# Kernel optimization log

Hardware: AMD Instinct MI355X
Metric: run time of the kernel (lower is better)

Reference implementation:

```python
import jax, jax.numpy as jnp
import numpy as np

# Model config (matches init_kwargs)
V, SMAX, D, DH, H, M, L = 32000, 512, 512, 64, 8, 2048, 6
B, S, T = 4, 512, 512
PAD = 0

_SPEC = [
    ("tok_emb", (V, D), "n"), ("pos_emb", (SMAX, D), "n"),
    ("enc_ln1_w", (L, D), "1"), ("enc_ln1_b", (L, D), "0"),
    ("enc_wq", (L, H, D, DH), "n"), ("enc_wk", (L, H, D, DH), "n"), ("enc_wv", (L, H, D, DH), "n"),
    ("enc_wo", (L, H * DH, D), "n"), ("enc_bo", (L, D), "0"),
    ("enc_ln2_w", (L, D), "1"), ("enc_ln2_b", (L, D), "0"),
    ("enc_w1", (L, D, M), "n"), ("enc_b1", (L, M), "0"),
    ("enc_w2", (L, M, D), "n"), ("enc_b2", (L, D), "0"),
    ("enc_lnf_w", (D,), "1"), ("enc_lnf_b", (D,), "0"),
    ("dec_ln1_w", (L, D), "1"), ("dec_ln1_b", (L, D), "0"),
    ("dec_wq_s", (L, H, D, DH), "n"), ("dec_wk_s", (L, H, D, DH), "n"), ("dec_wv_s", (L, H, D, DH), "n"),
    ("dec_wo_s", (L, H * DH, D), "n"), ("dec_bo_s", (L, D), "0"),
    ("dec_ln2_w", (L, D), "1"), ("dec_ln2_b", (L, D), "0"),
    ("dec_wq_c", (L, H, D, DH), "n"), ("dec_wk_c", (L, H, D, DH), "n"), ("dec_wv_c", (L, H, D, DH), "n"),
    ("dec_wo_c", (L, H * DH, D), "n"), ("dec_bo_c", (L, D), "0"),
    ("dec_ln3_w", (L, D), "1"), ("dec_ln3_b", (L, D), "0"),
    ("dec_w1", (L, D, M), "n"), ("dec_b1", (L, M), "0"),
    ("dec_w2", (L, M, D), "n"), ("dec_b2", (L, D), "0"),
    ("dec_lnf_w", (D,), "1"), ("dec_lnf_b", (D,), "0"),
    ("head_w", (D, V), "n"), ("head_b", (V,), "0"),
]


def setup_inputs() -> dict:
    key = jax.random.key(0)
    k1, k2, key = jax.random.split(key, 3)
    inp = {
        "tokens_source": jax.random.randint(k1, (B, S), 0, V),
        "tokens_destination": jax.random.randint(k2, (B, T), 0, V),
    }
    for name, shape, kind in _SPEC:
        if kind == "n":
            key, k = jax.random.split(key)
            inp[name] = jax.random.normal(k, shape, jnp.float32) * 0.02
        elif kind == "1":
            inp[name] = jnp.ones(shape, jnp.float32)
        else:
            inp[name] = jnp.zeros(shape, jnp.float32)
    return inp


def _ln(x, w, b):
    mu = x.mean(-1, keepdims=True)
    var = ((x - mu) ** 2).mean(-1, keepdims=True)
    return (x - mu) * jax.lax.rsqrt(var + 1e-5) * w + b


def _mha(xq, xkv, wq, wk, wv, wo, bo, mask):
    # wq/wk/wv: [H, D, dh]; wo: [H*dh, D]; mask: bool [B or 1, Sq, Sk] (broadcast over heads)
    q = jnp.einsum("bsd,hde->bhse", xq, wq)
    k = jnp.einsum("btd,hde->bhte", xkv, wk)
    v = jnp.einsum("btd,hde->bhte", xkv, wv)
    scores = jnp.einsum("bhse,bhte->bhst", q, k) / (DH ** 0.5)
    scores = jnp.where(mask[:, None], scores, -jnp.inf)
    w = jax.nn.softmax(scores, axis=-1)
    o = jnp.einsum("bhst,bhte->bhse", w, v)
    b_, _, s_, _ = o.shape
    o = o.transpose(0, 2, 1, 3).reshape(b_, s_, H * DH)  # concat heads (head 0 first)
    return o @ wo + bo


def _forward(src, dst, p):
    s_, t_ = src.shape[1], dst.shape[1]
    key_mask = (src != PAD)[:, None, :]                      # [B,1,S]: mask over source keys
    causal = jnp.tril(jnp.ones((t_, t_), bool))[None]        # [1,T,T]
    x = p["tok_emb"][src] + p["pos_emb"][:s_]
    for i in range(L):
        h = _ln(x, p["enc_ln1_w"][i], p["enc_ln1_b"][i])
        x = x + _mha(h, h, p["enc_wq"][i], p["enc_wk"][i], p["enc_wv"][i], p["enc_wo"][i], p["enc_bo"][i], key_mask)
        h = _ln(x, p["enc_ln2_w"][i], p["enc_ln2_b"][i])
        x = x + jax.nn.gelu(h @ p["enc_w1"][i] + p["enc_b1"][i], approximate=False) @ p["enc_w2"][i] + p["enc_b2"][i]
    xe = _ln(x, p["enc_lnf_w"], p["enc_lnf_b"])
    y = p["tok_emb"][dst] + p["pos_emb"][:t_]
    for i in range(L):
        h = _ln(y, p["dec_ln1_w"][i], p["dec_ln1_b"][i])
        y = y + _mha(h, h, p["dec_wq_s"][i], p["dec_wk_s"][i], p["dec_wv_s"][i], p["dec_wo_s"][i], p["dec_bo_s"][i], causal)
        h = _ln(y, p["dec_ln2_w"][i], p["dec_ln2_b"][i])
        y = y + _mha(h, xe, p["dec_wq_c"][i], p["dec_wk_c"][i], p["dec_wv_c"][i], p["dec_wo_c"][i], p["dec_bo_c"][i], key_mask)
        h = _ln(y, p["dec_ln3_w"][i], p["dec_ln3_b"][i])
        y = y + jax.nn.gelu(h @ p["dec_w1"][i] + p["dec_b1"][i], approximate=False) @ p["dec_w2"][i] + p["dec_b2"][i]
    yd = _ln(y, p["dec_lnf_w"], p["dec_lnf_b"])
    return yd @ p["head_w"] + p["head_b"]  # logits [B, T, V]


def reference(tokens_source, tokens_destination, tok_emb, pos_emb, enc_ln1_w, enc_ln1_b, enc_wq, enc_wk, enc_wv, enc_wo, enc_bo, enc_ln2_w, enc_ln2_b, enc_w1, enc_b1, enc_w2, enc_b2, enc_lnf_w, enc_lnf_b, dec_ln1_w, dec_ln1_b, dec_wq_s, dec_wk_s, dec_wv_s, dec_wo_s, dec_bo_s, dec_ln2_w, dec_ln2_b, dec_wq_c, dec_wk_c, dec_wv_c, dec_wo_c, dec_bo_c, dec_ln3_w, dec_ln3_b, dec_w1, dec_b1, dec_w2, dec_b2, dec_lnf_w, dec_lnf_b, head_w, head_b):
    p = {k: v for k, v in locals().items() if k not in ("tokens_source", "tokens_destination")}
    return _forward(tokens_source, tokens_destination, p)
```

## Files before the change

kernel.cpp:

```cpp
#include <hip/hip_runtime.h>
#include <math.h>


typedef __bf16 bf16;
typedef bf16  bf16x8 __attribute__((ext_vector_type(8)));
typedef float f32x4  __attribute__((ext_vector_type(4)));

#define DEV __device__ __forceinline__

DEV f32x4 mfma16(bf16x8 a, bf16x8 b, f32x4 c) {
  return __builtin_amdgcn_mfma_f32_16x16x32_bf16(a, b, c, 0, 0, 0);
}

DEV void async_copy16(const bf16* g, bf16* l) {
  __builtin_amdgcn_global_load_lds(
      (__attribute__((address_space(1))) void*)(g),
      (__attribute__((address_space(3))) void*)(l), 16, 0, 0);
}

__global__ __launch_bounds__(256) void tcast_kernel(
    const float* __restrict__ in, bf16* __restrict__ out, const int R, const int C,
    const long long oHi, const long long oLo, const int zdiv, const long long oOfs)
{
  __shared__ float tile[32][33];
  const int z = blockIdx.z;
  const long long zi = (long long)z * R * C;
  const long long zo = (long long)(z / zdiv) * oHi + (long long)(z % zdiv) * oLo + oOfs;
  const int c0 = blockIdx.x * 32, r0 = blockIdx.y * 32;
  const int tx = threadIdx.x, ty = threadIdx.y;
#pragma unroll
  for (int i = 0; i < 32; i += 8)
    tile[ty + i][tx] = in[zi + (long long)(r0 + ty + i) * C + c0 + tx];
  __syncthreads();
#pragma unroll
  for (int i = 0; i < 32; i += 8)
    out[zo + (long long)(c0 + ty + i) * R + r0 + tx] = (bf16)tile[tx][ty + i];
}

__global__ __launch_bounds__(128) void embed_kernel(
    const int* __restrict__ tok, const float* __restrict__ temb,
    const float* __restrict__ pemb, float* __restrict__ x)
{
  const int row  = blockIdx.x;
  const int sPos = row & 511;
  const int t    = tok[row];
  const int d    = threadIdx.x * 4;
  f32x4 a = *(const f32x4*)&temb[(long long)t * 512 + d];
  f32x4 p = *(const f32x4*)&pemb[(long long)sPos * 512 + d];
  *(f32x4*)&x[(long long)row * 512 + d] = a + p;
}

__global__ __launch_bounds__(64) void ln_kernel(
    const float* __restrict__ x, const float* __restrict__ w,
    const float* __restrict__ b, bf16* __restrict__ out)
{
  const int row = blockIdx.x;
  const int lane = threadIdx.x;
  const float* xr = x + (long long)row * 512;
  f32x4 a0 = *(const f32x4*)&xr[lane * 8];
  f32x4 a1 = *(const f32x4*)&xr[lane * 8 + 4];
  float s = 0.f, q = 0.f;
#pragma unroll
  for (int k = 0; k < 4; ++k) { s += a0[k] + a1[k]; q += a0[k]*a0[k] + a1[k]*a1[k]; }
#pragma unroll
  for (int m = 1; m < 64; m <<= 1) { s += __shfl_xor(s, m); q += __shfl_xor(q, m); }
  const float mean = s * (1.f / 512.f);
  const float var  = q * (1.f / 512.f) - mean * mean;
  const float rs   = rsqrtf(var + 1e-5f);
  f32x4 w0 = *(const f32x4*)&w[lane * 8], w1 = *(const f32x4*)&w[lane * 8 + 4];
  f32x4 b0 = *(const f32x4*)&b[lane * 8], b1 = *(const f32x4*)&b[lane * 8 + 4];
  bf16x8 o;
#pragma unroll
  for (int k = 0; k < 4; ++k) {
    o[k]     = (bf16)((a0[k] - mean) * rs * w0[k] + b0[k]);
    o[k + 4] = (bf16)((a1[k] - mean) * rs * w1[k] + b1[k]);
  }
  *(bf16x8*)&out[(long long)row * 512 + lane * 8] = o;
}

__global__ __launch_bounds__(256) void addln_kernel(
    const bf16* __restrict__ g, const float* __restrict__ bias,
    float* __restrict__ x, const float* __restrict__ w,
    const float* __restrict__ bb, bf16* __restrict__ out)
{
  const int row  = blockIdx.x * 4 + (threadIdx.x >> 6);
  const int lane = threadIdx.x & 63;
  const int c0   = lane * 8;
  float* xr = x + (long long)row * 512;
  f32x4 a0 = *(const f32x4*)&xr[c0];
  f32x4 a1 = *(const f32x4*)&xr[c0 + 4];
  bf16x8 gv = *(const bf16x8*)&g[(long long)row * 512 + c0];
  f32x4 bi0 = *(const f32x4*)&bias[c0], bi1 = *(const f32x4*)&bias[c0 + 4];
  float v[8];
#pragma unroll
  for (int k = 0; k < 4; ++k) {
    v[k]     = a0[k] + (float)gv[k]     + bi0[k];
    v[k + 4] = a1[k] + (float)gv[k + 4] + bi1[k];
  }
  *(f32x4*)&xr[c0]     = f32x4{v[0], v[1], v[2], v[3]};
  *(f32x4*)&xr[c0 + 4] = f32x4{v[4], v[5], v[6], v[7]};
  float s = 0.f, q = 0.f;
#pragma unroll
  for (int k = 0; k < 8; ++k) { s += v[k]; q += v[k] * v[k]; }
#pragma unroll
  for (int m = 1; m < 64; m <<= 1) { s += __shfl_xor(s, m); q += __shfl_xor(q, m); }
  const float mean = s * (1.f / 512.f);
  const float var  = q * (1.f / 512.f) - mean * mean;
  const float rs   = rsqrtf(var + 1e-5f);
  f32x4 w0 = *(const f32x4*)&w[c0], w1 = *(const f32x4*)&w[c0 + 4];
  f32x4 b0 = *(const f32x4*)&bb[c0], b1 = *(const f32x4*)&bb[c0 + 4];
  bf16x8 o;
#pragma unroll
  for (int k = 0; k < 4; ++k) {
    o[k]     = (bf16)((v[k] - mean) * rs * w0[k] + b0[k]);
    o[k + 4] = (bf16)((v[k + 4] - mean) * rs * w1[k] + b1[k]);
  }
  *(bf16x8*)&out[(long long)row * 512 + c0] = o;
}

template <int MODE>
__global__ __launch_bounds__(256) void attn_kernel(
    const bf16* __restrict__ Q, const bf16* __restrict__ K,
    const bf16* __restrict__ Vt, bf16* __restrict__ O,
    const int* __restrict__ srctok)
{
  __shared__ bf16 Qs[64 * 72];
  __shared__ bf16 Ks[128 * 72];
  __shared__ bf16 Vs[64 * 136];
  __shared__ bf16 Ps[4 * 16 * 132];
  __shared__ float Ms[512];

  const int bh = blockIdx.y;
  const int b  = bh >> 3;
  const int q0 = blockIdx.x * 64;
  const int tid = threadIdx.x;
  const int wv = tid >> 6, ln = tid & 63;
  const int lr = ln & 15, g = ln >> 4;
  const bf16* Qg = Q + ((long long)bh * 512 + q0) * 64;
  const bf16* Kg = K + (long long)bh * 512 * 64;
  const bf16* Vg = Vt + (long long)bh * 64 * 512;

  for (int i = tid; i < 512; i += 256) {
    const int r = i >> 3, c = (i & 7) * 8;
    *(uint4*)&Qs[r * 72 + c] = *(const uint4*)&Qg[r * 64 + c];
  }
  if (MODE == 0) {
    for (int i = tid; i < 512; i += 256)
      Ms[i] = (srctok[b * 512 + i] != 0) ? 0.f : -1e30f;
  }

  float m[4] = {-1e30f, -1e30f, -1e30f, -1e30f};
  float l[4] = {0.f, 0.f, 0.f, 0.f};
  f32x4 o[4] = {};

  const int ktEnd = (MODE == 1) ? (q0 + 64) : 512;
  bf16* Pw = Ps + wv * (16 * 132);

  for (int kt = 0; kt < ktEnd; kt += 128) {
    __syncthreads();
    for (int i = tid; i < 1024; i += 256) {
      const int r = i >> 3, c = (i & 7) * 8;
      *(uint4*)&Ks[r * 72 + c] = *(const uint4*)&Kg[(long long)(kt + r) * 64 + c];
    }
    for (int i = tid; i < 1024; i += 256) {
      const int r = i >> 4, c = (i & 15) * 8;
      *(uint4*)&Vs[r * 136 + c] = *(const uint4*)&Vg[(long long)r * 512 + kt + c];
    }
    __syncthreads();

    f32x4 sf[8] = {};
#pragma unroll
    for (int s = 0; s < 2; ++s) {
      const bf16x8 aq = *(const bf16x8*)&Qs[(wv * 16 + lr) * 72 + s * 32 + g * 8];
#pragma unroll
      for (int j = 0; j < 8; ++j) {
        const bf16x8 bk = *(const bf16x8*)&Ks[(j * 16 + lr) * 72 + s * 32 + g * 8];
        sf[j] = mfma16(aq, bk, sf[j]);
      }
    }
    float rm[4] = {-1e30f, -1e30f, -1e30f, -1e30f};
#pragma unroll
    for (int j = 0; j < 8; ++j) {
      if (MODE == 0) {
        const float ma = Ms[kt + j * 16 + lr];
#pragma unroll
        for (int r = 0; r < 4; ++r) sf[j][r] += ma;
      } else {
        const int key = kt + j * 16 + lr;
#pragma unroll
        for (int r = 0; r < 4; ++r) {
          const int qq = q0 + wv * 16 + g * 4 + r;
          if (key > qq) sf[j][r] = -1e30f;
        }
      }
#pragma unroll
      for (int r = 0; r < 4; ++r) rm[r] = fmaxf(rm[r], sf[j][r]);
    }
#pragma unroll
    for (int mk = 1; mk < 16; mk <<= 1)
#pragma unroll
      for (int r = 0; r < 4; ++r) rm[r] = fmaxf(rm[r], __shfl_xor(rm[r], mk));
    float al[4], ps[4] = {0.f, 0.f, 0.f, 0.f};
#pragma unroll
    for (int r = 0; r < 4; ++r) {
      const float mx = fmaxf(m[r], rm[r]);
      al[r] = __expf(m[r] - mx);
      m[r] = mx;
    }
#pragma unroll
    for (int j = 0; j < 8; ++j) {
#pragma unroll
      for (int r = 0; r < 4; ++r) {
        const float p = __expf(sf[j][r] - m[r]);
        ps[r] += p;
        Pw[(g * 4 + r) * 132 + j * 16 + lr] = (bf16)p;
      }
    }
#pragma unroll
    for (int mk = 1; mk < 16; mk <<= 1)
#pragma unroll
      for (int r = 0; r < 4; ++r) ps[r] += __shfl_xor(ps[r], mk);
#pragma unroll
    for (int r = 0; r < 4; ++r) l[r] = l[r] * al[r] + ps[r];
#pragma unroll
    for (int n = 0; n < 4; ++n)
#pragma unroll
      for (int r = 0; r < 4; ++r) o[n][r] *= al[r];
#pragma unroll
    for (int ks = 0; ks < 4; ++ks) {
      const bf16x8 ap = *(const bf16x8*)&Pw[lr * 132 + ks * 32 + g * 8];
#pragma unroll
      for (int n = 0; n < 4; ++n) {
        const bf16x8 bv = *(const bf16x8*)&Vs[(n * 16 + lr) * 136 + ks * 32 + g * 8];
        o[n] = mfma16(ap, bv, o[n]);
      }
    }
  }

#pragma unroll
  for (int r = 0; r < 4; ++r) {
    const float inv = 1.f / l[r];
    const long long gr = (long long)b * 512 + q0 + wv * 16 + g * 4 + r;
#pragma unroll
    for (int n = 0; n < 4; ++n)
      O[gr * 512 + (bh & 7) * 64 + n * 16 + lr] = (bf16)(o[n][r] * inv);
  }
}

template <int BM, int BN, int EPI>
__global__ __launch_bounds__(256) void gemm_kernel(
    const bf16* __restrict__ A, const bf16* __restrict__ Bw,
    void* __restrict__ Cc, const float* __restrict__ bias,
    const int K, const int lda, const int ldb, const int ldc,
    const long long sAz, const long long sBz,
    const long long sClo, const long long sChi, const int HB,
    const float scale)
{
  constexpr int BK = 64;
  __shared__ bf16 As[BM * BK];
  __shared__ bf16 Bs[BN * BK];
  constexpr int AISS = (BM * BK * 2) / 4096;
  constexpr int BISS = (BN * BK * 2) / 4096;

  const int z = blockIdx.z;
  const bf16* Az = A + (long long)z * sAz;
  const bf16* Bz = Bw + (long long)z * sBz;
  const long long cofs = (long long)(z % HB) * sClo + (long long)(z / HB) * sChi;

  const int tid  = threadIdx.x;
  const int wave = tid >> 6;
  const int lane = tid & 63;
  const int lr   = lane & 15;
  const int kg   = lane >> 4;

  const int m0 = blockIdx.x * BM;
  const int n0 = blockIdx.y * BN;

  constexpr int FM = BM / 32;
  constexpr int FN = BN / 32;
  const int wm = (wave >> 1) * (BM / 2);
  const int wn = (wave & 1) * (BN / 2);

  f32x4 acc[FM][FN] = {};

  for (int kt = 0; kt < K; kt += BK) {
#pragma unroll
    for (int i = 0; i < AISS; ++i) {
      const int o = i * 4096 + tid * 16;
      const int r = o >> 7;
      const int c = (o & 127) >> 1;
      async_copy16(Az + (long long)(m0 + r) * lda + kt + c, (bf16*)((char*)As + o));
    }
#pragma unroll
    for (int i = 0; i < BISS; ++i) {
      const int o = i * 4096 + tid * 16;
      const int r = o >> 7;
      const int c = (o & 127) >> 1;
      async_copy16(Bz + (long long)(n0 + r) * ldb + kt + c, (bf16*)((char*)Bs + o));
    }
    __syncthreads();
#pragma unroll
    for (int ks = 0; ks < 2; ++ks) {
      bf16x8 af[FM], bq[FN];
#pragma unroll
      for (int i = 0; i < FM; ++i)
        af[i] = *(const bf16x8*)&As[(wm + i * 16 + lr) * BK + ks * 32 + kg * 8];
#pragma unroll
      for (int j = 0; j < FN; ++j)
        bq[j] = *(const bf16x8*)&Bs[(wn + j * 16 + lr) * BK + ks * 32 + kg * 8];
#pragma unroll
      for (int i = 0; i < FM; ++i)
#pragma unroll
        for (int j = 0; j < FN; ++j)
          acc[i][j] = mfma16(af[i], bq[j], acc[i][j]);
    }
    __syncthreads();
  }

#pragma unroll
  for (int i = 0; i < FM; ++i) {
#pragma unroll
    for (int j = 0; j < FN; ++j) {
      const int gc = n0 + wn + j * 16 + lr;
#pragma unroll
      for (int r = 0; r < 4; ++r) {
        const int gr = m0 + wm + i * 16 + kg * 4 + r;
        const float v = acc[i][j][r];
        if constexpr (EPI == 0) {
          ((bf16*)Cc + cofs)[(long long)gr * ldc + gc] = (bf16)v;
        } else if constexpr (EPI == 3) {
          float t = v + bias[gc];
          t = 0.5f * t * (1.f + erff(t * 0.70710678118654752f));
          ((bf16*)Cc)[(long long)gr * ldc + gc] = (bf16)t;
        } else if constexpr (EPI == 4) {
          ((float*)Cc)[(long long)gr * ldc + gc] = v + bias[gc];
        } else if constexpr (EPI == 7) {
          const int sel = (gc >> 9) + (int)sClo;
          const int hh = (gc >> 6) & 7, ee = gc & 63;
          const int bb = gr >> 9, ss = gr & 511;
          bf16* base = (bf16*)Cc + (long long)sel * (2048 * 512);
          const float vv = (sel == 0) ? v * 0.125f : v;
          if (sel < 2) base[(((long long)(bb * 8 + hh) << 9) + ss) * 64 + ee] = (bf16)vv;
          else         base[(((long long)(bb * 8 + hh) << 6) + ee) * 512 + ss] = (bf16)vv;
        }
      }
    }
  }
}

extern "C" void kernel_launch(void* const* d_in, const int* in_sizes, int n_in,
                              void* d_out, int out_size, void* d_ws, size_t ws_size,
                              hipStream_t stream)
{
  const int*   tok_src   = (const int*)d_in[0];
  const int*   tok_dst   = (const int*)d_in[1];
  const float* tok_emb   = (const float*)d_in[2];
  const float* pos_emb   = (const float*)d_in[3];
  const float* enc_ln1_w = (const float*)d_in[4];
  const float* enc_ln1_b = (const float*)d_in[5];
  const float* enc_wq    = (const float*)d_in[6];
  const float* enc_wk    = (const float*)d_in[7];
  const float* enc_wv    = (const float*)d_in[8];
  const float* enc_wo    = (const float*)d_in[9];
  const float* enc_bo    = (const float*)d_in[10];
  const float* enc_ln2_w = (const float*)d_in[11];
  const float* enc_ln2_b = (const float*)d_in[12];
  const float* enc_w1    = (const float*)d_in[13];
  const float* enc_b1    = (const float*)d_in[14];
  const float* enc_w2    = (const float*)d_in[15];
  const float* enc_b2    = (const float*)d_in[16];
  const float* enc_lnf_w = (const float*)d_in[17];
  const float* enc_lnf_b = (const float*)d_in[18];
  const float* dec_ln1_w = (const float*)d_in[19];
  const float* dec_ln1_b = (const float*)d_in[20];
  const float* dec_wq_s  = (const float*)d_in[21];
  const float* dec_wk_s  = (const float*)d_in[22];
  const float* dec_wv_s  = (const float*)d_in[23];
  const float* dec_wo_s  = (const float*)d_in[24];
  const float* dec_bo_s  = (const float*)d_in[25];
  const float* dec_ln2_w = (const float*)d_in[26];
  const float* dec_ln2_b = (const float*)d_in[27];
  const float* dec_wq_c  = (const float*)d_in[28];
  const float* dec_wk_c  = (const float*)d_in[29];
  const float* dec_wv_c  = (const float*)d_in[30];
  const float* dec_wo_c  = (const float*)d_in[31];
  const float* dec_bo_c  = (const float*)d_in[32];
  const float* dec_ln3_w = (const float*)d_in[33];
  const float* dec_ln3_b = (const float*)d_in[34];
  const float* dec_w1    = (const float*)d_in[35];
  const float* dec_b1    = (const float*)d_in[36];
  const float* dec_w2    = (const float*)d_in[37];
  const float* dec_b2    = (const float*)d_in[38];
  const float* dec_lnf_w = (const float*)d_in[39];
  const float* dec_lnf_b = (const float*)d_in[40];
  const float* head_w    = (const float*)d_in[41];
  const float* head_b    = (const float*)d_in[42];
  float* outp = (float*)d_out;

  char* wp = (char*)d_ws;
  auto alloc = [&](size_t nbytes) -> char* {
    char* p = wp; wp += (nbytes + 255) & ~(size_t)255; return p;
  };
  const long long LQKV = 1536LL * 512;
  const long long LKV  = 1024LL * 512;
  const long long LSQ  = 512LL * 512;
  const long long LFF  = 2048LL * 512;

  bf16* tQKV_e = (bf16*)alloc((size_t)6 * LQKV * 2);
  bf16* tQKV_s = (bf16*)alloc((size_t)6 * LQKV * 2);
  bf16* tQ_c   = (bf16*)alloc((size_t)6 * LSQ * 2);
  bf16* tKV_c  = (bf16*)alloc((size_t)6 * LKV * 2);
  bf16* tWo_e  = (bf16*)alloc((size_t)6 * LSQ * 2);
  bf16* tWo_s  = (bf16*)alloc((size_t)6 * LSQ * 2);
  bf16* tWo_c  = (bf16*)alloc((size_t)6 * LSQ * 2);
  bf16* tW1_e  = (bf16*)alloc((size_t)6 * LFF * 2);
  bf16* tW2_e  = (bf16*)alloc((size_t)6 * LFF * 2);
  bf16* tW1_d  = (bf16*)alloc((size_t)6 * LFF * 2);
  bf16* tW2_d  = (bf16*)alloc((size_t)6 * LFF * 2);
  bf16* tHead  = (bf16*)alloc((size_t)32000 * 512 * 2);

  float* x   = (float*)alloc((size_t)2048 * 512 * 4);
  float* y   = (float*)alloc((size_t)2048 * 512 * 4);
  bf16*  h   = (bf16*)alloc((size_t)2048 * 512 * 2);
  bf16*  qkv = (bf16*)alloc((size_t)3 * 2048 * 512 * 2);
  bf16*  xe  = (bf16*)alloc((size_t)2048 * 512 * 2);
  bf16*  ob  = (bf16*)alloc((size_t)2048 * 512 * 2);
  bf16*  t0  = (bf16*)alloc((size_t)2048 * 512 * 2);
  bf16*  h1  = (bf16*)alloc((size_t)2048 * 2048 * 2);
  bf16*  yd  = (bf16*)alloc((size_t)2048 * 512 * 2);

  bf16* ql = qkv;
  bf16* kl = qkv + 2048 * 512;
  bf16* vt = qkv + 2 * 2048 * 512;

  const dim3 tb(32, 8);
  tcast_kernel<<<dim3(2, 16, 48), tb, 0, stream>>>(enc_wq, tQKV_e, 512, 64, LQKV, 32768, 8, 0);
  tcast_kernel<<<dim3(2, 16, 48), tb, 0, stream>>>(enc_wk, tQKV_e, 512, 64, LQKV, 32768, 8, 262144);
  tcast_kernel<<<dim3(2, 16, 48), tb, 0, stream>>>(enc_wv, tQKV_e, 512, 64, LQKV, 32768, 8, 524288);
  tcast_kernel<<<dim3(2, 16, 48), tb, 0, stream>>>(dec_wq_s, tQKV_s, 512, 64, LQKV, 32768, 8, 0);
  tcast_kernel<<<dim3(2, 16, 48), tb, 0, stream>>>(dec_wk_s, tQKV_s, 512, 64, LQKV, 32768, 8, 262144);
  tcast_kernel<<<dim3(2, 16, 48), tb, 0, stream>>>(dec_wv_s, tQKV_s, 512, 64, LQKV, 32768, 8, 524288);
  tcast_kernel<<<dim3(2, 16, 48), tb, 0, stream>>>(dec_wq_c, tQ_c, 512, 64, LSQ, 32768, 8, 0);
  tcast_kernel<<<dim3(2, 16, 48), tb, 0, stream>>>(dec_wk_c, tKV_c, 512, 64, LKV, 32768, 8, 0);
  tcast_kernel<<<dim3(2, 16, 48), tb, 0, stream>>>(dec_wv_c, tKV_c, 512, 64, LKV, 32768, 8, 262144);
  tcast_kernel<<<dim3(16, 16, 6), tb, 0, stream>>>(enc_wo, tWo_e, 512, 512, LSQ, 0, 1, 0);
  tcast_kernel<<<dim3(16, 16, 6), tb, 0, stream>>>(dec_wo_s, tWo_s, 512, 512, LSQ, 0, 1, 0);
  tcast_kernel<<<dim3(16, 16, 6), tb, 0, stream>>>(dec_wo_c, tWo_c, 512, 512, LSQ, 0, 1, 0);
  tcast_kernel<<<dim3(64, 16, 6), tb, 0, stream>>>(enc_w1, tW1_e, 512, 2048, LFF, 0, 1, 0);
  tcast_kernel<<<dim3(16, 64, 6), tb, 0, stream>>>(enc_w2, tW2_e, 2048, 512, LFF, 0, 1, 0);
  tcast_kernel<<<dim3(64, 16, 6), tb, 0, stream>>>(dec_w1, tW1_d, 512, 2048, LFF, 0, 1, 0);
  tcast_kernel<<<dim3(16, 64, 6), tb, 0, stream>>>(dec_w2, tW2_d, 2048, 512, LFF, 0, 1, 0);
  tcast_kernel<<<dim3(1000, 16, 1), tb, 0, stream>>>(head_w, tHead, 512, 32000, 0, 0, 1, 0);

  embed_kernel<<<2048, 128, 0, stream>>>(tok_src, tok_emb, pos_emb, x);
  ln_kernel<<<2048, 64, 0, stream>>>(x, enc_ln1_w, enc_ln1_b, h);
  for (int l = 0; l < 6; ++l) {
    gemm_kernel<128, 128, 7><<<dim3(16, 12, 1), 256, 0, stream>>>(
        h, tQKV_e + (size_t)l * LQKV, qkv, nullptr, 512, 512, 512, 0, 0, 0, 0, 0, 1, 1.f);
    attn_kernel<0><<<dim3(8, 32), 256, 0, stream>>>(ql, kl, vt, ob, tok_src);
    gemm_kernel<64, 64, 0><<<dim3(32, 8, 1), 256, 0, stream>>>(
        ob, tWo_e + (size_t)l * LSQ, t0, nullptr, 512, 512, 512, 512, 0, 0, 0, 0, 1, 1.f);
    addln_kernel<<<512, 256, 0, stream>>>(t0, enc_bo + l * 512, x,
        enc_ln2_w + l * 512, enc_ln2_b + l * 512, h);
    gemm_kernel<128, 128, 3><<<dim3(16, 16, 1), 256, 0, stream>>>(
        h, tW1_e + (size_t)l * LFF, h1, enc_b1 + l * 2048, 512, 512, 512, 2048, 0, 0, 0, 0, 1, 1.f);
    gemm_kernel<64, 64, 0><<<dim3(32, 8, 1), 256, 0, stream>>>(
        h1, tW2_e + (size_t)l * LFF, t0, nullptr, 2048, 2048, 2048, 512, 0, 0, 0, 0, 1, 1.f);
    const float* nw = (l < 5) ? enc_ln1_w + (l + 1) * 512 : enc_lnf_w;
    const float* nb = (l < 5) ? enc_ln1_b + (l + 1) * 512 : enc_lnf_b;
    addln_kernel<<<512, 256, 0, stream>>>(t0, enc_b2 + l * 512, x, nw, nb, (l < 5) ? h : xe);
  }

  embed_kernel<<<2048, 128, 0, stream>>>(tok_dst, tok_emb, pos_emb, y);
  ln_kernel<<<2048, 64, 0, stream>>>(y, dec_ln1_w, dec_ln1_b, h);
  for (int l = 0; l < 6; ++l) {
    gemm_kernel<128, 128, 7><<<dim3(16, 12, 1), 256, 0, stream>>>(
        h, tQKV_s + (size_t)l * LQKV, qkv, nullptr, 512, 512, 512, 0, 0, 0, 0, 0, 1, 1.f);
    attn_kernel<1><<<dim3(8, 32), 256, 0, stream>>>(ql, kl, vt, ob, nullptr);
    gemm_kernel<64, 64, 0><<<dim3(32, 8, 1), 256, 0, stream>>>(
        ob, tWo_s + (size_t)l * LSQ, t0, nullptr, 512, 512, 512, 512, 0, 0, 0, 0, 1, 1.f);
    addln_kernel<<<512, 256, 0, stream>>>(t0, dec_bo_s + l * 512, y,
        dec_ln2_w + l * 512, dec_ln2_b + l * 512, h);
    gemm_kernel<64, 64, 7><<<dim3(32, 8, 1), 256, 0, stream>>>(
        h, tQ_c + (size_t)l * LSQ, qkv, nullptr, 512, 512, 512, 0, 0, 0, 0, 0, 1, 1.f);
    gemm_kernel<128, 128, 7><<<dim3(16, 8, 1), 256, 0, stream>>>(
        xe, tKV_c + (size_t)l * LKV, qkv, nullptr, 512, 512, 512, 0, 0, 0, 1, 0, 1, 1.f);
    attn_kernel<0><<<dim3(8, 32), 256, 0, stream>>>(ql, kl, vt, ob, tok_src);
    gemm_kernel<64, 64, 0><<<dim3(32, 8, 1), 256, 0, stream>>>(
        ob, tWo_c + (size_t)l * LSQ, t0, nullptr, 512, 512, 512, 512, 0, 0, 0, 0, 1, 1.f);
    addln_kernel<<<512, 256, 0, stream>>>(t0, dec_bo_c + l * 512, y,
        dec_ln3_w + l * 512, dec_ln3_b + l * 512, h);
    gemm_kernel<128, 128, 3><<<dim3(16, 16, 1), 256, 0, stream>>>(
        h, tW1_d + (size_t)l * LFF, h1, dec_b1 + l * 2048, 512, 512, 512, 2048, 0, 0, 0, 0, 1, 1.f);
    gemm_kernel<64, 64, 0><<<dim3(32, 8, 1), 256, 0, stream>>>(
        h1, tW2_d + (size_t)l * LFF, t0, nullptr, 2048, 2048, 2048, 512, 0, 0, 0, 0, 1, 1.f);
    const float* nw = (l < 5) ? dec_ln1_w + (l + 1) * 512 : dec_lnf_w;
    const float* nb = (l < 5) ? dec_ln1_b + (l + 1) * 512 : dec_lnf_b;
    addln_kernel<<<512, 256, 0, stream>>>(t0, dec_b2 + l * 512, y, nw, nb, (l < 5) ? h : yd);
  }
  gemm_kernel<128, 128, 4><<<dim3(16, 250, 1), 256, 0, stream>>>(
      yd, tHead, outp, head_b, 512, 512, 512, 32000, 0, 0, 0, 0, 1, 1.f);
}
```

Baseline: 2.366 ms.

## Batch weight casts, fuse embed+LN, hoist cross-attn KV, retile attention

```diff
diff --git a/kernel.cpp b/kernel.cpp
--- a/kernel.cpp
+++ b/kernel.cpp
@@ -18,47 +18,55 @@
       (__attribute__((address_space(3))) void*)(l), 16, 0, 0);
 }
 
-__global__ __launch_bounds__(256) void tcast_kernel(
-    const float* __restrict__ in, bf16* __restrict__ out, const int R, const int C,
-    const long long oHi, const long long oLo, const int zdiv, const long long oOfs)
+struct TJob { const float* in; bf16* out; long long oHi, oLo, oOfs; int R, C, zdiv, tile0; };
+struct TJobs { TJob j[17]; };
+
+__global__ __launch_bounds__(256) void tcast_all(TJobs JJ, int njobs)
 {
   __shared__ float tile[32][33];
-  const int z = blockIdx.z;
-  const long long zi = (long long)z * R * C;
-  const long long zo = (long long)(z / zdiv) * oHi + (long long)(z % zdiv) * oLo + oOfs;
-  const int c0 = blockIdx.x * 32, r0 = blockIdx.y * 32;
-  const int tx = threadIdx.x, ty = threadIdx.y;
+  const int t = blockIdx.x;
+  int ji = 0;
+#pragma unroll
+  for (int k = 1; k < 17; ++k) if (k < njobs && JJ.j[k].tile0 <= t) ji = k;
+  const TJob J = JJ.j[ji];
+  const int rel  = t - J.tile0;
+  const int ntx  = J.C >> 5, nty = J.R >> 5;
+  const int perz = ntx * nty;
+  const int z    = rel / perz;
+  const int r2   = rel - z * perz;
+  const int bx   = r2 % ntx, by = r2 / ntx;
+
+  const long long zi = (long long)z * J.R * J.C;
+  const long long zo = (long long)(z / J.zdiv) * J.oHi + (long long)(z % J.zdiv) * J.oLo + J.oOfs;
+  const int c0 = bx * 32, r0 = by * 32;
+  const int tx = threadIdx.x & 31, ty = (threadIdx.x >> 5);
 #pragma unroll
   for (int i = 0; i < 32; i += 8)
-    tile[ty + i][tx] = in[zi + (long long)(r0 + ty + i) * C + c0 + tx];
+    tile[ty + i][tx] = J.in[zi + (long long)(r0 + ty + i) * J.C + c0 + tx];
   __syncthreads();
 #pragma unroll
   for (int i = 0; i < 32; i += 8)
-    out[zo + (long long)(c0 + ty + i) * R + r0 + tx] = (bf16)tile[tx][ty + i];
-}
-
-__global__ __launch_bounds__(128) void embed_kernel(
+    J.out[zo + (long long)(c0 + ty + i) * J.R + r0 + tx] = (bf16)tile[tx][ty + i];
+}
+
+__global__ __launch_bounds__(64) void embedln_kernel(
     const int* __restrict__ tok, const float* __restrict__ temb,
-    const float* __restrict__ pemb, float* __restrict__ x)
+    const float* __restrict__ pemb, float* __restrict__ x,
+    const float* __restrict__ w, const float* __restrict__ b,
+    bf16* __restrict__ out)
 {
   const int row  = blockIdx.x;
   const int sPos = row & 511;
   const int t    = tok[row];
-  const int d    = threadIdx.x * 4;
-  f32x4 a = *(const f32x4*)&temb[(long long)t * 512 + d];
-  f32x4 p = *(const f32x4*)&pemb[(long long)sPos * 512 + d];
-  *(f32x4*)&x[(long long)row * 512 + d] = a + p;
-}
-
-__global__ __launch_bounds__(64) void ln_kernel(
-    const float* __restrict__ x, const float* __restrict__ w,
-    const float* __restrict__ b, bf16* __restrict__ out)
-{
-  const int row = blockIdx.x;
   const int lane = threadIdx.x;
-  const float* xr = x + (long long)row * 512;
-  f32x4 a0 = *(const f32x4*)&xr[lane * 8];
-  f32x4 a1 = *(const f32x4*)&xr[lane * 8 + 4];
+  const int c0   = lane * 8;
+  f32x4 a0 = *(const f32x4*)&temb[(long long)t * 512 + c0];
+  f32x4 a1 = *(const f32x4*)&temb[(long long)t * 512 + c0 + 4];
+  f32x4 p0 = *(const f32x4*)&pemb[(long long)sPos * 512 + c0];
+  f32x4 p1 = *(const f32x4*)&pemb[(long long)sPos * 512 + c0 + 4];
+  a0 += p0; a1 += p1;
+  *(f32x4*)&x[(long long)row * 512 + c0]     = a0;
+  *(f32x4*)&x[(long long)row * 512 + c0 + 4] = a1;
   float s = 0.f, q = 0.f;
 #pragma unroll
   for (int k = 0; k < 4; ++k) { s += a0[k] + a1[k]; q += a0[k]*a0[k] + a1[k]*a1[k]; }
@@ -67,15 +75,15 @@
   const float mean = s * (1.f / 512.f);
   const float var  = q * (1.f / 512.f) - mean * mean;
   const float rs   = rsqrtf(var + 1e-5f);
-  f32x4 w0 = *(const f32x4*)&w[lane * 8], w1 = *(const f32x4*)&w[lane * 8 + 4];
-  f32x4 b0 = *(const f32x4*)&b[lane * 8], b1 = *(const f32x4*)&b[lane * 8 + 4];
+  f32x4 w0 = *(const f32x4*)&w[c0], w1 = *(const f32x4*)&w[c0 + 4];
+  f32x4 b0 = *(const f32x4*)&b[c0], b1 = *(const f32x4*)&b[c0 + 4];
   bf16x8 o;
 #pragma unroll
   for (int k = 0; k < 4; ++k) {
     o[k]     = (bf16)((a0[k] - mean) * rs * w0[k] + b0[k]);
     o[k + 4] = (bf16)((a1[k] - mean) * rs * w1[k] + b1[k]);
   }
-  *(bf16x8*)&out[(long long)row * 512 + lane * 8] = o;
+  *(bf16x8*)&out[(long long)row * 512 + c0] = o;
 }
 
 __global__ __launch_bounds__(256) void addln_kernel(
@@ -119,79 +127,51 @@
 }
 
 template <int MODE>
-__global__ __launch_bounds__(256) void attn_kernel(
+__global__ __launch_bounds__(64) void attn_kernel(
     const bf16* __restrict__ Q, const bf16* __restrict__ K,
     const bf16* __restrict__ Vt, bf16* __restrict__ O,
     const int* __restrict__ srctok)
 {
-  __shared__ bf16 Qs[64 * 72];
-  __shared__ bf16 Ks[128 * 72];
-  __shared__ bf16 Vs[64 * 136];
-  __shared__ bf16 Ps[4 * 16 * 132];
-  __shared__ float Ms[512];
-
+  __shared__ bf16 Pw[16 * 68];
   const int bh = blockIdx.y;
   const int b  = bh >> 3;
-  const int q0 = blockIdx.x * 64;
-  const int tid = threadIdx.x;
-  const int wv = tid >> 6, ln = tid & 63;
+  const int q0 = blockIdx.x * 16;
+  const int ln = threadIdx.x;
   const int lr = ln & 15, g = ln >> 4;
   const bf16* Qg = Q + ((long long)bh * 512 + q0) * 64;
   const bf16* Kg = K + (long long)bh * 512 * 64;
   const bf16* Vg = Vt + (long long)bh * 64 * 512;
-
-  for (int i = tid; i < 512; i += 256) {
-    const int r = i >> 3, c = (i & 7) * 8;
-    *(uint4*)&Qs[r * 72 + c] = *(const uint4*)&Qg[r * 64 + c];
-  }
-  if (MODE == 0) {
-    for (int i = tid; i < 512; i += 256)
-      Ms[i] = (srctok[b * 512 + i] != 0) ? 0.f : -1e30f;
-  }
+  const int* tkb = srctok + b * 512;
+
+  const bf16x8 aq0 = *(const bf16x8*)&Qg[lr * 64 + g * 8];
+  const bf16x8 aq1 = *(const bf16x8*)&Qg[lr * 64 + 32 + g * 8];
 
   float m[4] = {-1e30f, -1e30f, -1e30f, -1e30f};
   float l[4] = {0.f, 0.f, 0.f, 0.f};
   f32x4 o[4] = {};
 
-  const int ktEnd = (MODE == 1) ? (q0 + 64) : 512;
-  bf16* Pw = Ps + wv * (16 * 132);
-
-  for (int kt = 0; kt < ktEnd; kt += 128) {
-    __syncthreads();
-    for (int i = tid; i < 1024; i += 256) {
-      const int r = i >> 3, c = (i & 7) * 8;
-      *(uint4*)&Ks[r * 72 + c] = *(const uint4*)&Kg[(long long)(kt + r) * 64 + c];
-    }
-    for (int i = tid; i < 1024; i += 256) {
-      const int r = i >> 4, c = (i & 15) * 8;
-      *(uint4*)&Vs[r * 136 + c] = *(const uint4*)&Vg[(long long)r * 512 + kt + c];
-    }
-    __syncthreads();
-
-    f32x4 sf[8] = {};
-#pragma unroll
-    for (int s = 0; s < 2; ++s) {
-      const bf16x8 aq = *(const bf16x8*)&Qs[(wv * 16 + lr) * 72 + s * 32 + g * 8];
-#pragma unroll
-      for (int j = 0; j < 8; ++j) {
-        const bf16x8 bk = *(const bf16x8*)&Ks[(j * 16 + lr) * 72 + s * 32 + g * 8];
-        sf[j] = mfma16(aq, bk, sf[j]);
-      }
+  const int ktEnd = (MODE == 1) ? (q0 + 16) : 512;
+  for (int kt = 0; kt < ktEnd; kt += 64) {
+    f32x4 sf[4] = {};
+#pragma unroll
+    for (int j = 0; j < 4; ++j) {
+      const bf16x8 bk0 = *(const bf16x8*)&Kg[(long long)(kt + j * 16 + lr) * 64 + g * 8];
+      const bf16x8 bk1 = *(const bf16x8*)&Kg[(long long)(kt + j * 16 + lr) * 64 + 32 + g * 8];
+      sf[j] = mfma16(aq0, bk0, sf[j]);
+      sf[j] = mfma16(aq1, bk1, sf[j]);
     }
     float rm[4] = {-1e30f, -1e30f, -1e30f, -1e30f};
 #pragma unroll
-    for (int j = 0; j < 8; ++j) {
+    for (int j = 0; j < 4; ++j) {
       if (MODE == 0) {
-        const float ma = Ms[kt + j * 16 + lr];
-#pragma unroll
-        for (int r = 0; r < 4; ++r) sf[j][r] += ma;
+        const bool ok = (tkb[kt + j * 16 + lr] != 0);
+#pragma unroll
+        for (int r = 0; r < 4; ++r) if (!ok) sf[j][r] = -1e30f;
       } else {
         const int key = kt + j * 16 + lr;
 #pragma unroll
-        for (int r = 0; r < 4; ++r) {
-          const int qq = q0 + wv * 16 + g * 4 + r;
-          if (key > qq) sf[j][r] = -1e30f;
-        }
+        for (int r = 0; r < 4; ++r)
+          if (key > q0 + g * 4 + r) sf[j][r] = -1e30f;
       }
 #pragma unroll
       for (int r = 0; r < 4; ++r) rm[r] = fmaxf(rm[r], sf[j][r]);
@@ -208,12 +188,12 @@
       m[r] = mx;
     }
 #pragma unroll
-    for (int j = 0; j < 8; ++j) {
+    for (int j = 0; j < 4; ++j) {
 #pragma unroll
       for (int r = 0; r < 4; ++r) {
-        const float p = __expf(sf[j][r] - m[r]);
+        const float p = (sf[j][r] <= -1e29f) ? 0.f : __expf(sf[j][r] - m[r]);
         ps[r] += p;
-        Pw[(g * 4 + r) * 132 + j * 16 + lr] = (bf16)p;
+        Pw[(g * 4 + r) * 68 + j * 16 + lr] = (bf16)p;
       }
     }
 #pragma unroll
@@ -227,11 +207,11 @@
 #pragma unroll
       for (int r = 0; r < 4; ++r) o[n][r] *= al[r];
 #pragma unroll
-    for (int ks = 0; ks < 4; ++ks) {
-      const bf16x8 ap = *(const bf16x8*)&Pw[lr * 132 + ks * 32 + g * 8];
+    for (int ks = 0; ks < 2; ++ks) {
+      const bf16x8 ap = *(const bf16x8*)&Pw[lr * 68 + ks * 32 + g * 8];
 #pragma unroll
       for (int n = 0; n < 4; ++n) {
-        const bf16x8 bv = *(const bf16x8*)&Vs[(n * 16 + lr) * 136 + ks * 32 + g * 8];
+        const bf16x8 bv = *(const bf16x8*)&Vg[(long long)(n * 16 + lr) * 512 + kt + ks * 32 + g * 8];
         o[n] = mfma16(ap, bv, o[n]);
       }
     }
@@ -240,14 +220,14 @@
 #pragma unroll
   for (int r = 0; r < 4; ++r) {
     const float inv = 1.f / l[r];
-    const long long gr = (long long)b * 512 + q0 + wv * 16 + g * 4 + r;
+    const long long gr = (long long)b * 512 + q0 + g * 4 + r;
 #pragma unroll
     for (int n = 0; n < 4; ++n)
       O[gr * 512 + (bh & 7) * 64 + n * 16 + lr] = (bf16)(o[n][r] * inv);
   }
 }
 
-template <int BM, int BN, int EPI>
+template <int BM, int BN, int EPI, bool SWZ = false>
 __global__ __launch_bounds__(256) void gemm_kernel(
     const bf16* __restrict__ A, const bf16* __restrict__ Bw,
     void* __restrict__ Cc, const float* __restrict__ bias,
@@ -273,8 +253,17 @@
   const int lr   = lane & 15;
   const int kg   = lane >> 4;
 
-  const int m0 = blockIdx.x * BM;
-  const int n0 = blockIdx.y * BN;
+  int bx = blockIdx.x, by = blockIdx.y;
+  if constexpr (SWZ) {
+    const int nx = gridDim.x;
+    const int nwg = nx * gridDim.y;
+    const int id = by * nx + bx;
+    const int chunk = nwg >> 3;
+    const int swz = (id & 7) * chunk + (id >> 3);
+    bx = swz % nx; by = swz / nx;
+  }
+  const int m0 = bx * BM;
+  const int n0 = by * BN;
 
   constexpr int FM = BM / 32;
   constexpr int FN = BN / 32;
@@ -333,15 +322,22 @@
           t = 0.5f * t * (1.f + erff(t * 0.70710678118654752f));
           ((bf16*)Cc)[(long long)gr * ldc + gc] = (bf16)t;
         } else if constexpr (EPI == 4) {
-          ((float*)Cc)[(long long)gr * ldc + gc] = v + bias[gc];
+          __builtin_nontemporal_store(v + bias[gc], &((float*)Cc)[(long long)gr * ldc + gc]);
         } else if constexpr (EPI == 7) {
-          const int sel = (gc >> 9) + (int)sClo;
+          const int sel = gc >> 9;
           const int hh = (gc >> 6) & 7, ee = gc & 63;
           const int bb = gr >> 9, ss = gr & 511;
           bf16* base = (bf16*)Cc + (long long)sel * (2048 * 512);
           const float vv = (sel == 0) ? v * 0.125f : v;
           if (sel < 2) base[(((long long)(bb * 8 + hh) << 9) + ss) * 64 + ee] = (bf16)vv;
           else         base[(((long long)(bb * 8 + hh) << 6) + ee) * 512 + ss] = (bf16)vv;
+        } else if constexpr (EPI == 8) {
+          const int sel = gc >> 9;
+          const int hh = (gc >> 6) & 7, ee = gc & 63;
+          const int bb = gr >> 9, ss = gr & 511;
+          bf16* base = (bf16*)Cc + (long long)z * sChi + (long long)sel * (2048 * 512);
+          if (sel == 0) base[(((long long)(bb * 8 + hh) << 9) + ss) * 64 + ee] = (bf16)v;
+          else          base[(((long long)(bb * 8 + hh) << 6) + ee) * 512 + ss] = (bf16)v;
         }
       }
     }
@@ -405,6 +401,7 @@
   const long long LKV  = 1024LL * 512;
   const long long LSQ  = 512LL * 512;
   const long long LFF  = 2048LL * 512;
+  const long long KVST = 2LL * 2048 * 512;
 
   bf16* tQKV_e = (bf16*)alloc((size_t)6 * LQKV * 2);
   bf16* tQKV_s = (bf16*)alloc((size_t)6 * LQKV * 2);
@@ -424,6 +421,7 @@
   bf16*  h   = (bf16*)alloc((size_t)2048 * 512 * 2);
   bf16*  qkv = (bf16*)alloc((size_t)3 * 2048 * 512 * 2);
   bf16*  xe  = (bf16*)alloc((size_t)2048 * 512 * 2);
+  bf16*  kvc = (bf16*)alloc((size_t)6 * KVST * 2);
   bf16*  ob  = (bf16*)alloc((size_t)2048 * 512 * 2);
   bf16*  t0  = (bf16*)alloc((size_t)2048 * 512 * 2);
   bf16*  h1  = (bf16*)alloc((size_t)2048 * 2048 * 2);
@@ -433,31 +431,36 @@
   bf16* kl = qkv + 2048 * 512;
   bf16* vt = qkv + 2 * 2048 * 512;
 
-  const dim3 tb(32, 8);
-  tcast_kernel<<<dim3(2, 16, 48), tb, 0, stream>>>(enc_wq, tQKV_e, 512, 64, LQKV, 32768, 8, 0);
-  tcast_kernel<<<dim3(2, 16, 48), tb, 0, stream>>>(enc_wk, tQKV_e, 512, 64, LQKV, 32768, 8, 262144);
-  tcast_kernel<<<dim3(2, 16, 48), tb, 0, stream>>>(enc_wv, tQKV_e, 512, 64, LQKV, 32768, 8, 524288);
-  tcast_kernel<<<dim3(2, 16, 48), tb, 0, stream>>>(dec_wq_s, tQKV_s, 512, 64, LQKV, 32768, 8, 0);
-  tcast_kernel<<<dim3(2, 16, 48), tb, 0, stream>>>(dec_wk_s, tQKV_s, 512, 64, LQKV, 32768, 8, 262144);
-  tcast_kernel<<<dim3(2, 16, 48), tb, 0, stream>>>(dec_wv_s, tQKV_s, 512, 64, LQKV, 32768, 8, 524288);
-  tcast_kernel<<<dim3(2, 16, 48), tb, 0, stream>>>(dec_wq_c, tQ_c, 512, 64, LSQ, 32768, 8, 0);
-  tcast_kernel<<<dim3(2, 16, 48), tb, 0, stream>>>(dec_wk_c, tKV_c, 512, 64, LKV, 32768, 8, 0);
-  tcast_kernel<<<dim3(2, 16, 48), tb, 0, stream>>>(dec_wv_c, tKV_c, 512, 64, LKV, 32768, 8, 262144);
-  tcast_kernel<<<dim3(16, 16, 6), tb, 0, stream>>>(enc_wo, tWo_e, 512, 512, LSQ, 0, 1, 0);
-  tcast_kernel<<<dim3(16, 16, 6), tb, 0, stream>>>(dec_wo_s, tWo_s, 512, 512, LSQ, 0, 1, 0);
-  tcast_kernel<<<dim3(16, 16, 6), tb, 0, stream>>>(dec_wo_c, tWo_c, 512, 512, LSQ, 0, 1, 0);
-  tcast_kernel<<<dim3(64, 16, 6), tb, 0, stream>>>(enc_w1, tW1_e, 512, 2048, LFF, 0, 1, 0);
-  tcast_kernel<<<dim3(16, 64, 6), tb, 0, stream>>>(enc_w2, tW2_e, 2048, 512, LFF, 0, 1, 0);
-  tcast_kernel<<<dim3(64, 16, 6), tb, 0, stream>>>(dec_w1, tW1_d, 512, 2048, LFF, 0, 1, 0);
-  tcast_kernel<<<dim3(16, 64, 6), tb, 0, stream>>>(dec_w2, tW2_d, 2048, 512, LFF, 0, 1, 0);
-  tcast_kernel<<<dim3(1000, 16, 1), tb, 0, stream>>>(head_w, tHead, 512, 32000, 0, 0, 1, 0);
-
-  embed_kernel<<<2048, 128, 0, stream>>>(tok_src, tok_emb, pos_emb, x);
-  ln_kernel<<<2048, 64, 0, stream>>>(x, enc_ln1_w, enc_ln1_b, h);
+  TJobs JJ; int nt = 0, nj = 0;
+  auto addjob = [&](const float* in, bf16* out, int R, int C,
+                    long long oHi, long long oLo, int zdiv, long long oOfs, int nz) {
+    JJ.j[nj] = TJob{in, out, oHi, oLo, oOfs, R, C, zdiv, nt};
+    nt += (C / 32) * (R / 32) * nz; ++nj;
+  };
+  addjob(enc_wq,   tQKV_e, 512, 64,   LQKV, 32768, 8, 0,      48);
+  addjob(enc_wk,   tQKV_e, 512, 64,   LQKV, 32768, 8, 262144, 48);
+  addjob(enc_wv,   tQKV_e, 512, 64,   LQKV, 32768, 8, 524288, 48);
+  addjob(dec_wq_s, tQKV_s, 512, 64,   LQKV, 32768, 8, 0,      48);
+  addjob(dec_wk_s, tQKV_s, 512, 64,   LQKV, 32768, 8, 262144, 48);
+  addjob(dec_wv_s, tQKV_s, 512, 64,   LQKV, 32768, 8, 524288, 48);
+  addjob(dec_wq_c, tQ_c,   512, 64,   LSQ,  32768, 8, 0,      48);
+  addjob(dec_wk_c, tKV_c,  512, 64,   LKV,  32768, 8, 0,      48);
+  addjob(dec_wv_c, tKV_c,  512, 64,   LKV,  32768, 8, 262144, 48);
+  addjob(enc_wo,   tWo_e,  512, 512,  LSQ,  0, 1, 0, 6);
+  addjob(dec_wo_s, tWo_s,  512, 512,  LSQ,  0, 1, 0, 6);
+  addjob(dec_wo_c, tWo_c,  512, 512,  LSQ,  0, 1, 0, 6);
+  addjob(enc_w1,   tW1_e,  512, 2048, LFF,  0, 1, 0, 6);
+  addjob(enc_w2,   tW2_e,  2048, 512, LFF,  0, 1, 0, 6);
+  addjob(dec_w1,   tW1_d,  512, 2048, LFF,  0, 1, 0, 6);
+  addjob(dec_w2,   tW2_d,  2048, 512, LFF,  0, 1, 0, 6);
+  addjob(head_w,   tHead,  512, 32000, 0,   0, 1, 0, 1);
+  tcast_all<<<nt, 256, 0, stream>>>(JJ, nj);
+
+  embedln_kernel<<<2048, 64, 0, stream>>>(tok_src, tok_emb, pos_emb, x, enc_ln1_w, enc_ln1_b, h);
   for (int l = 0; l < 6; ++l) {
     gemm_kernel<128, 128, 7><<<dim3(16, 12, 1), 256, 0, stream>>>(
         h, tQKV_e + (size_t)l * LQKV, qkv, nullptr, 512, 512, 512, 0, 0, 0, 0, 0, 1, 1.f);
-    attn_kernel<0><<<dim3(8, 32), 256, 0, stream>>>(ql, kl, vt, ob, tok_src);
+    attn_kernel<0><<<dim3(32, 32), 64, 0, stream>>>(ql, kl, vt, ob, tok_src);
     gemm_kernel<64, 64, 0><<<dim3(32, 8, 1), 256, 0, stream>>>(
         ob, tWo_e + (size_t)l * LSQ, t0, nullptr, 512, 512, 512, 512, 0, 0, 0, 0, 1, 1.f);
     addln_kernel<<<512, 256, 0, stream>>>(t0, enc_bo + l * 512, x,
@@ -471,21 +474,22 @@
     addln_kernel<<<512, 256, 0, stream>>>(t0, enc_b2 + l * 512, x, nw, nb, (l < 5) ? h : xe);
   }
 
-  embed_kernel<<<2048, 128, 0, stream>>>(tok_dst, tok_emb, pos_emb, y);
-  ln_kernel<<<2048, 64, 0, stream>>>(y, dec_ln1_w, dec_ln1_b, h);
+  gemm_kernel<128, 128, 8><<<dim3(16, 8, 6), 256, 0, stream>>>(
+      xe, tKV_c, kvc, nullptr, 512, 512, 512, 0, 0, LKV, 0, KVST, 1, 1.f);
+
+  embedln_kernel<<<2048, 64, 0, stream>>>(tok_dst, tok_emb, pos_emb, y, dec_ln1_w, dec_ln1_b, h);
   for (int l = 0; l < 6; ++l) {
     gemm_kernel<128, 128, 7><<<dim3(16, 12, 1), 256, 0, stream>>>(
         h, tQKV_s + (size_t)l * LQKV, qkv, nullptr, 512, 512, 512, 0, 0, 0, 0, 0, 1, 1.f);
-    attn_kernel<1><<<dim3(8, 32), 256, 0, stream>>>(ql, kl, vt, ob, nullptr);
+    attn_kernel<1><<<dim3(32, 32), 64, 0, stream>>>(ql, kl, vt, ob, nullptr);
     gemm_kernel<64, 64, 0><<<dim3(32, 8, 1), 256, 0, stream>>>(
         ob, tWo_s + (size_t)l * LSQ, t0, nullptr, 512, 512, 512, 512, 0, 0, 0, 0, 1, 1.f);
     addln_kernel<<<512, 256, 0, stream>>>(t0, dec_bo_s + l * 512, y,
         dec_ln2_w + l * 512, dec_ln2_b + l * 512, h);
     gemm_kernel<64, 64, 7><<<dim3(32, 8, 1), 256, 0, stream>>>(
         h, tQ_c + (size_t)l * LSQ, qkv, nullptr, 512, 512, 512, 0, 0, 0, 0, 0, 1, 1.f);
-    gemm_kernel<128, 128, 7><<<dim3(16, 8, 1), 256, 0, stream>>>(
-        xe, tKV_c + (size_t)l * LKV, qkv, nullptr, 512, 512, 512, 0, 0, 0, 1, 0, 1, 1.f);
-    attn_kernel<0><<<dim3(8, 32), 256, 0, stream>>>(ql, kl, vt, ob, tok_src);
+    attn_kernel<0><<<dim3(32, 32), 64, 0, stream>>>(
+        ql, kvc + (size_t)l * KVST, kvc + (size_t)l * KVST + 2048 * 512, ob, tok_src);
     gemm_kernel<64, 64, 0><<<dim3(32, 8, 1), 256, 0, stream>>>(
         ob, tWo_c + (size_t)l * LSQ, t0, nullptr, 512, 512, 512, 512, 0, 0, 0, 0, 1, 1.f);
     addln_kernel<<<512, 256, 0, stream>>>(t0, dec_bo_c + l * 512, y,
@@ -498,6 +502,6 @@
     const float* nb = (l < 5) ? dec_ln1_b + (l + 1) * 512 : dec_lnf_b;
     addln_kernel<<<512, 256, 0, stream>>>(t0, dec_b2 + l * 512, y, nw, nb, (l < 5) ? h : yd);
   }
-  gemm_kernel<128, 128, 4><<<dim3(16, 250, 1), 256, 0, stream>>>(
+  gemm_kernel<128, 128, 4, true><<<dim3(16, 250, 1), 256, 0, stream>>>(
       yd, tHead, outp, head_b, 512, 512, 512, 32000, 0, 0, 0, 0, 1, 1.f);
 }
```

New measurement: 2.252 ms. 1.05x faster.
